# Optimization experiments

Hardware: AMD Instinct MI355X
Metric: run time of the kernel (lower is better)

The kernel has to match this reference:

```python
import jax, jax.numpy as jnp
import numpy as np


def setup_inputs() -> dict:
    key = jax.random.key(0)
    k1, k2 = jax.random.split(key)
    x = jax.random.normal(k1, (32, 112, 112, 64), dtype=jnp.float32)
    kernels = jax.random.normal(k2, (3, 3, 64, 128), dtype=jnp.float32) * 0.05
    biases = jnp.zeros((128,), dtype=jnp.float32)
    return {"x": x, "kernels": kernels, "biases": biases}


def reference(x, kernels, biases):
    # Stride-1 VALID cross-correlation, NHWC input, HWIO kernel -> NHWC output.
    # Matches the original's per-pixel sum(patch * kernel) over all input channels.
    out = jax.lax.conv_general_dilated(
        x, kernels,
        window_strides=(1, 1),
        padding="VALID",
        dimension_numbers=("NHWC", "HWIO", "NHWC"),
    )
    out = out + biases  # broadcast over (B, H_out, W_out, F)
    return jax.nn.relu(out)  # activation=relu per init_kwargs
```

## Files before the change

kernel.cpp:

```cpp
#include <hip/hip_runtime.h>
#include <hip/hip_bf16.h>

typedef __attribute__((ext_vector_type(4))) float f32x4;
typedef __attribute__((ext_vector_type(8))) short bf16x8;
typedef __attribute__((ext_vector_type(8))) unsigned short u16x8;
typedef __attribute__((ext_vector_type(4))) unsigned int u32x4;

#define HH 112
#define WW 112
#define CIN 64
#define COUT 128
#define HOUT 110
#define WOUT 110
#define MTOT 387200
#define NWG 3025
#define NXCD 8
#define XNE 25690112

__device__ __forceinline__ unsigned short f2bf(float f) {
  unsigned int x = __float_as_uint(f);
  x += 0x7fffu + ((x >> 16) & 1u);
  return (unsigned short)(x >> 16);
}

__device__ __forceinline__ unsigned int cvt2(float lo, float hi) {
  union { __hip_bfloat162 h; unsigned int u; } cv;
  cv.h = __float22bfloat162_rn(float2{lo, hi});
  return cv.u;
}

__device__ __forceinline__ void gload16(const unsigned short* g, unsigned short* l) {
  __builtin_amdgcn_global_load_lds(
      (const __attribute__((address_space(1))) void*)g,
      (__attribute__((address_space(3))) void*)l, 16, 0, 0);
}

__global__ __launch_bounds__(256)
void cvt_x_kernel(const float* __restrict__ x, unsigned short* __restrict__ xb) {
  const int t = blockIdx.x * 256 + threadIdx.x;
  const f32x4* s = (const f32x4*)x + (size_t)t * 2;
  f32x4 a = s[0], b = s[1];
  u32x4 v;
  v[0] = cvt2(a[0], a[1]); v[1] = cvt2(a[2], a[3]);
  v[2] = cvt2(b[0], b[1]); v[3] = cvt2(b[2], b[3]);
  ((u32x4*)xb)[t] = v;
}

__global__ void prepack_b_kernel(const float* __restrict__ kern,
                                 unsigned short* __restrict__ bt) {
  int idx = blockIdx.x * 256 + threadIdx.x;
  if (idx >= 9 * 8192) return;
  int tap = idx >> 13;
  int rem = idx & 8191;
  int co = rem >> 6;
  int e = rem & 63;
  int ci = ((e * 2) ^ ((co & 7) << 4)) >> 1;
  bt[idx] = f2bf(kern[(tap * 64 + ci) * COUT + co]);
}

__global__ __launch_bounds__(512, 4)
void conv_dma_kernel(const unsigned short* __restrict__ xb,
                     const unsigned short* __restrict__ bt,
                     const float* __restrict__ bias,
                     float* __restrict__ out) {
  __shared__ __align__(16) unsigned short As[2][8192];
  __shared__ __align__(16) unsigned short Bs[2][8192];

  const int tid = threadIdx.x;
  const int lane = tid & 63;
  const int wid = tid >> 6;

  const int bid = blockIdx.x;
  const int q = NWG / NXCD, r = NWG % NXCD;
  const int xcd = bid % NXCD, i8 = bid / NXCD;
  const int wg = (xcd < r ? xcd * (q + 1) : r * (q + 1) + (xcd - r) * q) + i8;
  const int m0 = wg * 128;

  int aoff[2];
  const int obase = wid * 2048 + lane * 16;
#pragma unroll
  for (int j = 0; j < 2; ++j) {
    const int o = obase + j * 1024;
    const int rr = o >> 7;
    const int ss = (o >> 4) & 7;
    const int sp = ss ^ (rr & 7);
    const int m = m0 + rr;
    const int wo = m % WOUT;
    const int t1 = m / WOUT;
    const int ho = t1 % HOUT;
    const int bb = t1 / HOUT;
    aoff[j] = (((bb * HH) + ho) * WW + wo) * CIN + sp * 8;
  }
  const int ldsw0 = wid * 1024;
  const int ldsw1 = wid * 1024 + 512;
  const int blin0 = ldsw0 + lane * 8;
  const int blin1 = ldsw1 + lane * 8;

  const int wm = wid >> 1;
  const int wn = wid & 1;
  const int l16 = lane & 15;
  const int lk = lane >> 4;
  const int swzR = (l16 & 7) << 4;

  const int aroff0 = (wm * 32 + 0 + l16) * 64;
  const int aroff1 = (wm * 32 + 16 + l16) * 64;
  const int broff0 = (wn * 64 + 0 + l16) * 64;
  const int broff1 = (wn * 64 + 16 + l16) * 64;
  const int broff2 = (wn * 64 + 32 + l16) * 64;
  const int broff3 = (wn * 64 + 48 + l16) * 64;

  f32x4 acc[2][4];
#pragma unroll
  for (int i = 0; i < 2; ++i)
#pragma unroll
    for (int j = 0; j < 4; ++j)
      acc[i][j] = (f32x4){0.f, 0.f, 0.f, 0.f};

  gload16(xb + aoff[0], &As[0][ldsw0]);
  gload16(xb + aoff[1], &As[0][ldsw1]);
  gload16(bt + blin0, &Bs[0][ldsw0]);
  gload16(bt + blin1, &Bs[0][ldsw1]);
  __syncthreads();

#pragma unroll
  for (int kk = 0; kk < 9; ++kk) {
    const int cur = kk & 1;
    const int nxt = cur ^ 1;

    if (kk < 8) {
      const int kn = kk + 1;
      const int kh = kn / 3;
      const int kw = kn - kh * 3;
      const int te = (kh * WW + kw) * CIN;
      const int tb = kn * 8192;
      gload16(xb + aoff[0] + te, &As[nxt][ldsw0]);
      gload16(xb + aoff[1] + te, &As[nxt][ldsw1]);
      gload16(bt + tb + blin0, &Bs[nxt][ldsw0]);
      gload16(bt + tb + blin1, &Bs[nxt][ldsw1]);
    }

    const unsigned short* Ac = As[cur];
    const unsigned short* Bc = Bs[cur];
#pragma unroll
    for (int ks = 0; ks < 2; ++ks) {
      const int cbs = ((ks * 64 + lk * 16) ^ swzR) >> 1;
      bf16x8 a0 = *(const bf16x8*)(Ac + aroff0 + cbs);
      bf16x8 a1 = *(const bf16x8*)(Ac + aroff1 + cbs);
      bf16x8 b0 = *(const bf16x8*)(Bc + broff0 + cbs);
      bf16x8 b1 = *(const bf16x8*)(Bc + broff1 + cbs);
      bf16x8 b2 = *(const bf16x8*)(Bc + broff2 + cbs);
      bf16x8 b3 = *(const bf16x8*)(Bc + broff3 + cbs);
      acc[0][0] = __builtin_amdgcn_mfma_f32_16x16x32_bf16(a0, b0, acc[0][0], 0, 0, 0);
      acc[0][1] = __builtin_amdgcn_mfma_f32_16x16x32_bf16(a0, b1, acc[0][1], 0, 0, 0);
      acc[0][2] = __builtin_amdgcn_mfma_f32_16x16x32_bf16(a0, b2, acc[0][2], 0, 0, 0);
      acc[0][3] = __builtin_amdgcn_mfma_f32_16x16x32_bf16(a0, b3, acc[0][3], 0, 0, 0);
      acc[1][0] = __builtin_amdgcn_mfma_f32_16x16x32_bf16(a1, b0, acc[1][0], 0, 0, 0);
      acc[1][1] = __builtin_amdgcn_mfma_f32_16x16x32_bf16(a1, b1, acc[1][1], 0, 0, 0);
      acc[1][2] = __builtin_amdgcn_mfma_f32_16x16x32_bf16(a1, b2, acc[1][2], 0, 0, 0);
      acc[1][3] = __builtin_amdgcn_mfma_f32_16x16x32_bf16(a1, b3, acc[1][3], 0, 0, 0);
    }

    __syncthreads();
  }

  const int ncol = wn * 64 + l16;
  const float bv0 = bias[ncol + 0];
  const float bv1 = bias[ncol + 16];
  const float bv2 = bias[ncol + 32];
  const float bv3 = bias[ncol + 48];
  const int mrow0 = m0 + wm * 32 + lk * 4;
#pragma unroll
  for (int mf = 0; mf < 2; ++mf) {
#pragma unroll
    for (int j = 0; j < 4; ++j) {
      const int row = mrow0 + mf * 16 + j;
      float* orow = out + (size_t)row * COUT + ncol;
      orow[0]  = fmaxf(acc[mf][0][j] + bv0, 0.f);
      orow[16] = fmaxf(acc[mf][1][j] + bv1, 0.f);
      orow[32] = fmaxf(acc[mf][2][j] + bv2, 0.f);
      orow[48] = fmaxf(acc[mf][3][j] + bv3, 0.f);
    }
  }
}

__global__ __launch_bounds__(512)
void conv_fallback_kernel(const float* __restrict__ x,
                          const float* __restrict__ kern,
                          const float* __restrict__ bias,
                          float* __restrict__ out) {
  __shared__ __align__(16) unsigned short As[2][128 * 64];
  __shared__ __align__(16) unsigned short Bs[2][128 * 64];

  const int tid = threadIdx.x;
  const int m0 = blockIdx.x * 128;

  const int sr = tid >> 2;
  const int sc = tid & 3;
  const int m = m0 + sr;
  const int wo = m % WOUT;
  const int t1 = m / WOUT;
  const int ho = t1 % HOUT;
  const int b = t1 / HOUT;
  const float* xrow = x + (((b * HH) + ho) * WW + wo) * CIN + sc * 16;
  const int swzS = (sr & 7) << 4;
  const int awoff0 = sr * 64 + ((((sc * 32) + 0) ^ swzS) >> 1);
  const int awoff1 = sr * 64 + ((((sc * 32) + 16) ^ swzS) >> 1);

  const int bci = tid >> 3;
  const int bco = (tid & 7) * 16;

  const int lane = tid & 63;
  const int wid = tid >> 6;
  const int wm = wid >> 1;
  const int wn = wid & 1;
  const int l16 = lane & 15;
  const int lk = lane >> 4;
  const int swzR = (l16 & 7) << 4;

  const int aroff0 = (wm * 32 + 0 + l16) * 64;
  const int aroff1 = (wm * 32 + 16 + l16) * 64;
  const int broff0 = (wn * 64 + 0 + l16) * 64;
  const int broff1 = (wn * 64 + 16 + l16) * 64;
  const int broff2 = (wn * 64 + 32 + l16) * 64;
  const int broff3 = (wn * 64 + 48 + l16) * 64;

  f32x4 acc[2][4];
#pragma unroll
  for (int i = 0; i < 2; ++i)
#pragma unroll
    for (int j = 0; j < 4; ++j)
      acc[i][j] = (f32x4){0.f, 0.f, 0.f, 0.f};

  {
    f32x4 f0 = *(const f32x4*)(xrow + 0);
    f32x4 f1 = *(const f32x4*)(xrow + 4);
    f32x4 f2 = *(const f32x4*)(xrow + 8);
    f32x4 f3 = *(const f32x4*)(xrow + 12);
    u32x4 va, vb;
    va[0] = cvt2(f0[0], f0[1]); va[1] = cvt2(f0[2], f0[3]);
    va[2] = cvt2(f1[0], f1[1]); va[3] = cvt2(f1[2], f1[3]);
    vb[0] = cvt2(f2[0], f2[1]); vb[1] = cvt2(f2[2], f2[3]);
    vb[2] = cvt2(f3[0], f3[1]); vb[3] = cvt2(f3[2], f3[3]);
    *(u32x4*)(As[0] + awoff0) = va;
    *(u32x4*)(As[0] + awoff1) = vb;
    const float* kslab = kern + bci * COUT + bco;
    f32x4 g0 = *(const f32x4*)(kslab + 0);
    f32x4 g1 = *(const f32x4*)(kslab + 4);
    f32x4 g2 = *(const f32x4*)(kslab + 8);
    f32x4 g3 = *(const f32x4*)(kslab + 12);
#pragma unroll
    for (int j = 0; j < 4; ++j) {
      int c0 = bco + j;
      Bs[0][c0 * 64 + (((bci * 2) ^ ((c0 & 7) << 4)) >> 1)] = f2bf(g0[j]);
      int c1 = bco + 4 + j;
      Bs[0][c1 * 64 + (((bci * 2) ^ ((c1 & 7) << 4)) >> 1)] = f2bf(g1[j]);
      int c2 = bco + 8 + j;
      Bs[0][c2 * 64 + (((bci * 2) ^ ((c2 & 7) << 4)) >> 1)] = f2bf(g2[j]);
      int c3 = bco + 12 + j;
      Bs[0][c3 * 64 + (((bci * 2) ^ ((c3 & 7) << 4)) >> 1)] = f2bf(g3[j]);
    }
  }

#pragma unroll
  for (int kk = 0; kk < 9; ++kk) {
    const int cur = kk & 1;
    const int nxt = cur ^ 1;

    f32x4 g0, g1, g2, g3;
    f32x4 h0, h1, h2, h3;
    if (kk < 8) {
      const int kn = kk + 1;
      const int kh2 = kn / 3;
      const int kw2 = kn - kh2 * 3;
      const float* src = xrow + (kh2 * WW + kw2) * CIN;
      g0 = *(const f32x4*)(src + 0);
      g1 = *(const f32x4*)(src + 4);
      g2 = *(const f32x4*)(src + 8);
      g3 = *(const f32x4*)(src + 12);
      const float* kslab = kern + (kn * 64 + bci) * COUT + bco;
      h0 = *(const f32x4*)(kslab + 0);
      h1 = *(const f32x4*)(kslab + 4);
      h2 = *(const f32x4*)(kslab + 8);
      h3 = *(const f32x4*)(kslab + 12);
    }

    __syncthreads();

    const unsigned short* Ac = As[cur];
    const unsigned short* Bc = Bs[cur];
#pragma unroll
    for (int ks = 0; ks < 2; ++ks) {
      const int cbs = ((ks * 64 + lk * 16) ^ swzR) >> 1;
      bf16x8 a0 = *(const bf16x8*)(Ac + aroff0 + cbs);
      bf16x8 a1 = *(const bf16x8*)(Ac + aroff1 + cbs);
      bf16x8 b0 = *(const bf16x8*)(Bc + broff0 + cbs);
      bf16x8 b1 = *(const bf16x8*)(Bc + broff1 + cbs);
      bf16x8 b2 = *(const bf16x8*)(Bc + broff2 + cbs);
      bf16x8 b3 = *(const bf16x8*)(Bc + broff3 + cbs);
      acc[0][0] = __builtin_amdgcn_mfma_f32_16x16x32_bf16(a0, b0, acc[0][0], 0, 0, 0);
      acc[0][1] = __builtin_amdgcn_mfma_f32_16x16x32_bf16(a0, b1, acc[0][1], 0, 0, 0);
      acc[0][2] = __builtin_amdgcn_mfma_f32_16x16x32_bf16(a0, b2, acc[0][2], 0, 0, 0);
      acc[0][3] = __builtin_amdgcn_mfma_f32_16x16x32_bf16(a0, b3, acc[0][3], 0, 0, 0);
      acc[1][0] = __builtin_amdgcn_mfma_f32_16x16x32_bf16(a1, b0, acc[1][0], 0, 0, 0);
      acc[1][1] = __builtin_amdgcn_mfma_f32_16x16x32_bf16(a1, b1, acc[1][1], 0, 0, 0);
      acc[1][2] = __builtin_amdgcn_mfma_f32_16x16x32_bf16(a1, b2, acc[1][2], 0, 0, 0);
      acc[1][3] = __builtin_amdgcn_mfma_f32_16x16x32_bf16(a1, b3, acc[1][3], 0, 0, 0);
    }

    if (kk < 8) {
      u32x4 va, vb;
      va[0] = cvt2(g0[0], g0[1]); va[1] = cvt2(g0[2], g0[3]);
      va[2] = cvt2(g1[0], g1[1]); va[3] = cvt2(g1[2], g1[3]);
      vb[0] = cvt2(g2[0], g2[1]); vb[1] = cvt2(g2[2], g2[3]);
      vb[2] = cvt2(g3[0], g3[1]); vb[3] = cvt2(g3[2], g3[3]);
      *(u32x4*)(As[nxt] + awoff0) = va;
      *(u32x4*)(As[nxt] + awoff1) = vb;
#pragma unroll
      for (int j = 0; j < 4; ++j) {
        int c0 = bco + j;
        Bs[nxt][c0 * 64 + (((bci * 2) ^ ((c0 & 7) << 4)) >> 1)] = f2bf(h0[j]);
        int c1 = bco + 4 + j;
        Bs[nxt][c1 * 64 + (((bci * 2) ^ ((c1 & 7) << 4)) >> 1)] = f2bf(h1[j]);
        int c2 = bco + 8 + j;
        Bs[nxt][c2 * 64 + (((bci * 2) ^ ((c2 & 7) << 4)) >> 1)] = f2bf(h2[j]);
        int c3 = bco + 12 + j;
        Bs[nxt][c3 * 64 + (((bci * 2) ^ ((c3 & 7) << 4)) >> 1)] = f2bf(h3[j]);
      }
    }
  }

  const int ncol = wn * 64 + l16;
  const float bv0 = bias[ncol + 0];
  const float bv1 = bias[ncol + 16];
  const float bv2 = bias[ncol + 32];
  const float bv3 = bias[ncol + 48];
  const int mrow0 = m0 + wm * 32 + lk * 4;
#pragma unroll
  for (int mf = 0; mf < 2; ++mf) {
#pragma unroll
    for (int j = 0; j < 4; ++j) {
      const int row = mrow0 + mf * 16 + j;
      float* orow = out + (size_t)row * COUT + ncol;
      orow[0]  = fmaxf(acc[mf][0][j] + bv0, 0.f);
      orow[16] = fmaxf(acc[mf][1][j] + bv1, 0.f);
      orow[32] = fmaxf(acc[mf][2][j] + bv2, 0.f);
      orow[48] = fmaxf(acc[mf][3][j] + bv3, 0.f);
    }
  }
}

extern "C" void kernel_launch(void* const* d_in, const int* in_sizes, int n_in,
                              void* d_out, int out_size, void* d_ws, size_t ws_size,
                              hipStream_t stream) {
  const float* x = (const float*)d_in[0];
  const float* kern = (const float*)d_in[1];
  const float* bias = (const float*)d_in[2];
  float* out = (float*)d_out;

  const size_t xb_bytes = (size_t)XNE * 2;
  const size_t bt_bytes = 9 * 8192 * 2;
  if (d_ws != nullptr && ws_size >= xb_bytes + bt_bytes) {
    unsigned short* xb = (unsigned short*)d_ws;
    unsigned short* bt = xb + XNE;
    cvt_x_kernel<<<12544, 256, 0, stream>>>(x, xb);
    prepack_b_kernel<<<288, 256, 0, stream>>>(kern, bt);
    conv_dma_kernel<<<NWG, 512, 0, stream>>>(xb, bt, bias, out);
  } else {
    conv_fallback_kernel<<<NWG, 512, 0, stream>>>(x, kern, bias, out);
  }
}
```

Before: 110.1 us.

## Halve workgroup to 4 waves, each computing a 64x64 tile

The conv workgroup drops from 8 waves to 4 while keeping the same 128x128 output tile, so each wave now computes 64x64 (4x4 MFMA fragments) instead of 32x64. Each thread issues twice as many async global-to-LDS loads per tap. This raises per-wave register reuse of LDS fragments and cuts LDS read traffic per MFMA. The cost is more accumulator registers per thread and fewer waves to hide latency, with launch bounds changed to 256 threads and 2 blocks.

```diff
diff --git a/kernel.cpp b/kernel.cpp
--- a/kernel.cpp
+++ b/kernel.cpp
@@ -58,7 +58,7 @@
   bt[idx] = f2bf(kern[(tap * 64 + ci) * COUT + co]);
 }
 
-__global__ __launch_bounds__(512, 4)
+__global__ __launch_bounds__(256, 2)
 void conv_dma_kernel(const unsigned short* __restrict__ xb,
                      const unsigned short* __restrict__ bt,
                      const float* __restrict__ bias,
@@ -76,11 +76,10 @@
   const int wg = (xcd < r ? xcd * (q + 1) : r * (q + 1) + (xcd - r) * q) + i8;
   const int m0 = wg * 128;
 
-  int aoff[2];
-  const int obase = wid * 2048 + lane * 16;
-#pragma unroll
-  for (int j = 0; j < 2; ++j) {
-    const int o = obase + j * 1024;
+  int aoff[4];
+#pragma unroll
+  for (int j = 0; j < 4; ++j) {
+    const int o = wid * 4096 + j * 1024 + lane * 16;
     const int rr = o >> 7;
     const int ss = (o >> 4) & 7;
     const int sp = ss ^ (rr & 7);
@@ -91,10 +90,12 @@
     const int bb = t1 / HOUT;
     aoff[j] = (((bb * HH) + ho) * WW + wo) * CIN + sp * 8;
   }
-  const int ldsw0 = wid * 1024;
-  const int ldsw1 = wid * 1024 + 512;
-  const int blin0 = ldsw0 + lane * 8;
-  const int blin1 = ldsw1 + lane * 8;
+  int ldsw[4], blin[4];
+#pragma unroll
+  for (int j = 0; j < 4; ++j) {
+    ldsw[j] = wid * 2048 + j * 512;
+    blin[j] = ldsw[j] + lane * 8;
+  }
 
   const int wm = wid >> 1;
   const int wn = wid & 1;
@@ -102,24 +103,25 @@
   const int lk = lane >> 4;
   const int swzR = (l16 & 7) << 4;
 
-  const int aroff0 = (wm * 32 + 0 + l16) * 64;
-  const int aroff1 = (wm * 32 + 16 + l16) * 64;
-  const int broff0 = (wn * 64 + 0 + l16) * 64;
-  const int broff1 = (wn * 64 + 16 + l16) * 64;
-  const int broff2 = (wn * 64 + 32 + l16) * 64;
-  const int broff3 = (wn * 64 + 48 + l16) * 64;
-
-  f32x4 acc[2][4];
-#pragma unroll
-  for (int i = 0; i < 2; ++i)
+  int ar[4], br[4];
+#pragma unroll
+  for (int f = 0; f < 4; ++f) {
+    ar[f] = (wm * 64 + f * 16 + l16) * 64;
+    br[f] = (wn * 64 + f * 16 + l16) * 64;
+  }
+
+  f32x4 acc[4][4];
+#pragma unroll
+  for (int i = 0; i < 4; ++i)
 #pragma unroll
     for (int j = 0; j < 4; ++j)
       acc[i][j] = (f32x4){0.f, 0.f, 0.f, 0.f};
 
-  gload16(xb + aoff[0], &As[0][ldsw0]);
-  gload16(xb + aoff[1], &As[0][ldsw1]);
-  gload16(bt + blin0, &Bs[0][ldsw0]);
-  gload16(bt + blin1, &Bs[0][ldsw1]);
+#pragma unroll
+  for (int j = 0; j < 4; ++j) {
+    gload16(xb + aoff[j], &As[0][ldsw[j]]);
+    gload16(bt + blin[j], &Bs[0][ldsw[j]]);
+  }
   __syncthreads();
 
 #pragma unroll
@@ -133,10 +135,11 @@
       const int kw = kn - kh * 3;
       const int te = (kh * WW + kw) * CIN;
       const int tb = kn * 8192;
-      gload16(xb + aoff[0] + te, &As[nxt][ldsw0]);
-      gload16(xb + aoff[1] + te, &As[nxt][ldsw1]);
-      gload16(bt + tb + blin0, &Bs[nxt][ldsw0]);
-      gload16(bt + tb + blin1, &Bs[nxt][ldsw1]);
+#pragma unroll
+      for (int j = 0; j < 4; ++j) {
+        gload16(xb + aoff[j] + te, &As[nxt][ldsw[j]]);
+        gload16(bt + tb + blin[j], &Bs[nxt][ldsw[j]]);
+      }
     }
 
     const unsigned short* Ac = As[cur];
@@ -144,12 +147,14 @@
 #pragma unroll
     for (int ks = 0; ks < 2; ++ks) {
       const int cbs = ((ks * 64 + lk * 16) ^ swzR) >> 1;
-      bf16x8 a0 = *(const bf16x8*)(Ac + aroff0 + cbs);
-      bf16x8 a1 = *(const bf16x8*)(Ac + aroff1 + cbs);
-      bf16x8 b0 = *(const bf16x8*)(Bc + broff0 + cbs);
-      bf16x8 b1 = *(const bf16x8*)(Bc + broff1 + cbs);
-      bf16x8 b2 = *(const bf16x8*)(Bc + broff2 + cbs);
-      bf16x8 b3 = *(const bf16x8*)(Bc + broff3 + cbs);
+      bf16x8 a0 = *(const bf16x8*)(Ac + ar[0] + cbs);
+      bf16x8 a1 = *(const bf16x8*)(Ac + ar[1] + cbs);
+      bf16x8 a2 = *(const bf16x8*)(Ac + ar[2] + cbs);
+      bf16x8 a3 = *(const bf16x8*)(Ac + ar[3] + cbs);
+      bf16x8 b0 = *(const bf16x8*)(Bc + br[0] + cbs);
+      bf16x8 b1 = *(const bf16x8*)(Bc + br[1] + cbs);
+      bf16x8 b2 = *(const bf16x8*)(Bc + br[2] + cbs);
+      bf16x8 b3 = *(const bf16x8*)(Bc + br[3] + cbs);
       acc[0][0] = __builtin_amdgcn_mfma_f32_16x16x32_bf16(a0, b0, acc[0][0], 0, 0, 0);
       acc[0][1] = __builtin_amdgcn_mfma_f32_16x16x32_bf16(a0, b1, acc[0][1], 0, 0, 0);
       acc[0][2] = __builtin_amdgcn_mfma_f32_16x16x32_bf16(a0, b2, acc[0][2], 0, 0, 0);
@@ -158,6 +163,14 @@
       acc[1][1] = __builtin_amdgcn_mfma_f32_16x16x32_bf16(a1, b1, acc[1][1], 0, 0, 0);
       acc[1][2] = __builtin_amdgcn_mfma_f32_16x16x32_bf16(a1, b2, acc[1][2], 0, 0, 0);
       acc[1][3] = __builtin_amdgcn_mfma_f32_16x16x32_bf16(a1, b3, acc[1][3], 0, 0, 0);
+      acc[2][0] = __builtin_amdgcn_mfma_f32_16x16x32_bf16(a2, b0, acc[2][0], 0, 0, 0);
+      acc[2][1] = __builtin_amdgcn_mfma_f32_16x16x32_bf16(a2, b1, acc[2][1], 0, 0, 0);
+      acc[2][2] = __builtin_amdgcn_mfma_f32_16x16x32_bf16(a2, b2, acc[2][2], 0, 0, 0);
+      acc[2][3] = __builtin_amdgcn_mfma_f32_16x16x32_bf16(a2, b3, acc[2][3], 0, 0, 0);
+      acc[3][0] = __builtin_amdgcn_mfma_f32_16x16x32_bf16(a3, b0, acc[3][0], 0, 0, 0);
+      acc[3][1] = __builtin_amdgcn_mfma_f32_16x16x32_bf16(a3, b1, acc[3][1], 0, 0, 0);
+      acc[3][2] = __builtin_amdgcn_mfma_f32_16x16x32_bf16(a3, b2, acc[3][2], 0, 0, 0);
+      acc[3][3] = __builtin_amdgcn_mfma_f32_16x16x32_bf16(a3, b3, acc[3][3], 0, 0, 0);
     }
 
     __syncthreads();
@@ -168,13 +181,12 @@
   const float bv1 = bias[ncol + 16];
   const float bv2 = bias[ncol + 32];
   const float bv3 = bias[ncol + 48];
-  const int mrow0 = m0 + wm * 32 + lk * 4;
-#pragma unroll
-  for (int mf = 0; mf < 2; ++mf) {
+#pragma unroll
+  for (int mf = 0; mf < 4; ++mf) {
+    const int rbase = m0 + wm * 64 + mf * 16 + lk * 4;
 #pragma unroll
     for (int j = 0; j < 4; ++j) {
-      const int row = mrow0 + mf * 16 + j;
-      float* orow = out + (size_t)row * COUT + ncol;
+      float* orow = out + (size_t)(rbase + j) * COUT + ncol;
       orow[0]  = fmaxf(acc[mf][0][j] + bv0, 0.f);
       orow[16] = fmaxf(acc[mf][1][j] + bv1, 0.f);
       orow[32] = fmaxf(acc[mf][2][j] + bv2, 0.f);
@@ -364,7 +376,7 @@
     unsigned short* bt = xb + XNE;
     cvt_x_kernel<<<12544, 256, 0, stream>>>(x, xb);
     prepack_b_kernel<<<288, 256, 0, stream>>>(kern, bt);
-    conv_dma_kernel<<<NWG, 512, 0, stream>>>(xb, bt, bias, out);
+    conv_dma_kernel<<<NWG, 256, 0, stream>>>(xb, bt, bias, out);
   } else {
     conv_fallback_kernel<<<NWG, 512, 0, stream>>>(x, kern, bias, out);
   }
```

Measured after the change: 117.4 us. +6.7%, slower.

## Load weight fragments directly from global into registers instead of LDS

Applied to the files above, without the earlier changes.

The weight (B) tile is no longer staged through shared memory. Each lane loads its MFMA B fragments straight from the prepacked global buffer into double-buffered registers, and the prepack now uses an unswizzled layout. This halves LDS usage and removes the LDS reads for B, which could allow higher occupancy, and it also drops the final barrier. The cost is more VGPRs (32 extra bf16x8 registers) and uncoalesced-ish per-lane global loads that rely on L2/L1 hits, which may raise register pressure under launch_bounds(512,4).

```diff
diff --git a/kernel.cpp b/kernel.cpp
--- a/kernel.cpp
+++ b/kernel.cpp
@@ -53,8 +53,7 @@
   int tap = idx >> 13;
   int rem = idx & 8191;
   int co = rem >> 6;
-  int e = rem & 63;
-  int ci = ((e * 2) ^ ((co & 7) << 4)) >> 1;
+  int ci = rem & 63;
   bt[idx] = f2bf(kern[(tap * 64 + ci) * COUT + co]);
 }
 
@@ -64,7 +63,6 @@
                      const float* __restrict__ bias,
                      float* __restrict__ out) {
   __shared__ __align__(16) unsigned short As[2][8192];
-  __shared__ __align__(16) unsigned short Bs[2][8192];
 
   const int tid = threadIdx.x;
   const int lane = tid & 63;
@@ -82,8 +80,7 @@
   for (int j = 0; j < 2; ++j) {
     const int o = obase + j * 1024;
     const int rr = o >> 7;
-    const int ss = (o >> 4) & 7;
-    const int sp = ss ^ (rr & 7);
+    const int sp = ((o >> 4) & 7) ^ (rr & 7);
     const int m = m0 + rr;
     const int wo = m % WOUT;
     const int t1 = m / WOUT;
@@ -93,8 +90,6 @@
   }
   const int ldsw0 = wid * 1024;
   const int ldsw1 = wid * 1024 + 512;
-  const int blin0 = ldsw0 + lane * 8;
-  const int blin1 = ldsw1 + lane * 8;
 
   const int wm = wid >> 1;
   const int wn = wid & 1;
@@ -104,10 +99,8 @@
 
   const int aroff0 = (wm * 32 + 0 + l16) * 64;
   const int aroff1 = (wm * 32 + 16 + l16) * 64;
-  const int broff0 = (wn * 64 + 0 + l16) * 64;
-  const int broff1 = (wn * 64 + 16 + l16) * 64;
-  const int broff2 = (wn * 64 + 32 + l16) * 64;
-  const int broff3 = (wn * 64 + 48 + l16) * 64;
+
+  const unsigned short* bq_base = bt + (wn * 64 + l16) * 64 + lk * 8;
 
   f32x4 acc[2][4];
 #pragma unroll
@@ -116,10 +109,15 @@
     for (int j = 0; j < 4; ++j)
       acc[i][j] = (f32x4){0.f, 0.f, 0.f, 0.f};
 
+  bf16x8 bq[2][2][4];
+
   gload16(xb + aoff[0], &As[0][ldsw0]);
   gload16(xb + aoff[1], &As[0][ldsw1]);
-  gload16(bt + blin0, &Bs[0][ldsw0]);
-  gload16(bt + blin1, &Bs[0][ldsw1]);
+#pragma unroll
+  for (int f = 0; f < 4; ++f)
+#pragma unroll
+    for (int ks = 0; ks < 2; ++ks)
+      bq[0][ks][f] = *(const bf16x8*)(bq_base + f * 1024 + ks * 32);
   __syncthreads();
 
 #pragma unroll
@@ -132,35 +130,33 @@
       const int kh = kn / 3;
       const int kw = kn - kh * 3;
       const int te = (kh * WW + kw) * CIN;
-      const int tb = kn * 8192;
       gload16(xb + aoff[0] + te, &As[nxt][ldsw0]);
       gload16(xb + aoff[1] + te, &As[nxt][ldsw1]);
-      gload16(bt + tb + blin0, &Bs[nxt][ldsw0]);
-      gload16(bt + tb + blin1, &Bs[nxt][ldsw1]);
+      const unsigned short* bsrc = bq_base + kn * 8192;
+#pragma unroll
+      for (int f = 0; f < 4; ++f)
+#pragma unroll
+        for (int ks = 0; ks < 2; ++ks)
+          bq[nxt][ks][f] = *(const bf16x8*)(bsrc + f * 1024 + ks * 32);
     }
 
     const unsigned short* Ac = As[cur];
-    const unsigned short* Bc = Bs[cur];
 #pragma unroll
     for (int ks = 0; ks < 2; ++ks) {
       const int cbs = ((ks * 64 + lk * 16) ^ swzR) >> 1;
       bf16x8 a0 = *(const bf16x8*)(Ac + aroff0 + cbs);
       bf16x8 a1 = *(const bf16x8*)(Ac + aroff1 + cbs);
-      bf16x8 b0 = *(const bf16x8*)(Bc + broff0 + cbs);
-      bf16x8 b1 = *(const bf16x8*)(Bc + broff1 + cbs);
-      bf16x8 b2 = *(const bf16x8*)(Bc + broff2 + cbs);
-      bf16x8 b3 = *(const bf16x8*)(Bc + broff3 + cbs);
-      acc[0][0] = __builtin_amdgcn_mfma_f32_16x16x32_bf16(a0, b0, acc[0][0], 0, 0, 0);
-      acc[0][1] = __builtin_amdgcn_mfma_f32_16x16x32_bf16(a0, b1, acc[0][1], 0, 0, 0);
-      acc[0][2] = __builtin_amdgcn_mfma_f32_16x16x32_bf16(a0, b2, acc[0][2], 0, 0, 0);
-      acc[0][3] = __builtin_amdgcn_mfma_f32_16x16x32_bf16(a0, b3, acc[0][3], 0, 0, 0);
-      acc[1][0] = __builtin_amdgcn_mfma_f32_16x16x32_bf16(a1, b0, acc[1][0], 0, 0, 0);
-      acc[1][1] = __builtin_amdgcn_mfma_f32_16x16x32_bf16(a1, b1, acc[1][1], 0, 0, 0);
-      acc[1][2] = __builtin_amdgcn_mfma_f32_16x16x32_bf16(a1, b2, acc[1][2], 0, 0, 0);
-      acc[1][3] = __builtin_amdgcn_mfma_f32_16x16x32_bf16(a1, b3, acc[1][3], 0, 0, 0);
-    }
-
-    __syncthreads();
+      acc[0][0] = __builtin_amdgcn_mfma_f32_16x16x32_bf16(a0, bq[cur][ks][0], acc[0][0], 0, 0, 0);
+      acc[0][1] = __builtin_amdgcn_mfma_f32_16x16x32_bf16(a0, bq[cur][ks][1], acc[0][1], 0, 0, 0);
+      acc[0][2] = __builtin_amdgcn_mfma_f32_16x16x32_bf16(a0, bq[cur][ks][2], acc[0][2], 0, 0, 0);
+      acc[0][3] = __builtin_amdgcn_mfma_f32_16x16x32_bf16(a0, bq[cur][ks][3], acc[0][3], 0, 0, 0);
+      acc[1][0] = __builtin_amdgcn_mfma_f32_16x16x32_bf16(a1, bq[cur][ks][0], acc[1][0], 0, 0, 0);
+      acc[1][1] = __builtin_amdgcn_mfma_f32_16x16x32_bf16(a1, bq[cur][ks][1], acc[1][1], 0, 0, 0);
+      acc[1][2] = __builtin_amdgcn_mfma_f32_16x16x32_bf16(a1, bq[cur][ks][2], acc[1][2], 0, 0, 0);
+      acc[1][3] = __builtin_amdgcn_mfma_f32_16x16x32_bf16(a1, bq[cur][ks][3], acc[1][3], 0, 0, 0);
+    }
+
+    if (kk < 8) __syncthreads();
   }
 
   const int ncol = wn * 64 + l16;
@@ -366,6 +362,6 @@
     prepack_b_kernel<<<288, 256, 0, stream>>>(kern, bt);
     conv_dma_kernel<<<NWG, 512, 0, stream>>>(xb, bt, bias, out);
   } else {
-    conv_fallback_kernel<<<NWG, 512, 0, stream>>>(x, kern, bias, out);
-  }
-}
+    conv_fallback_kernel<<<3025, 512, 0, stream>>>(x, kern, bias, out);
+  }
+}
```

New measurement: 249.5 us. +126.7%, slower.

## Triple-buffer A tiles with vmcnt-based waits and a single barrier per tap

Applied to the files above, without the earlier changes.

The A (activation) tile ring grows from two LDS buffers to three, so the loads for tap k+2 are issued while tap k computes. The B prefetch stays double-buffered. The per-iteration __syncthreads pair becomes one explicit s_waitcnt vmcnt plus s_barrier, which keeps later prefetches in flight instead of draining all outstanding loads. The cost is more LDS per block (48KB), which could lower occupancy, and correctness now depends on the async load counter ordering being right.

```diff
diff --git a/kernel.cpp b/kernel.cpp
--- a/kernel.cpp
+++ b/kernel.cpp
@@ -63,7 +63,7 @@
                      const unsigned short* __restrict__ bt,
                      const float* __restrict__ bias,
                      float* __restrict__ out) {
-  __shared__ __align__(16) unsigned short As[2][8192];
+  __shared__ __align__(16) unsigned short As[3][8192];
   __shared__ __align__(16) unsigned short Bs[2][8192];
 
   const int tid = threadIdx.x;
@@ -82,8 +82,7 @@
   for (int j = 0; j < 2; ++j) {
     const int o = obase + j * 1024;
     const int rr = o >> 7;
-    const int ss = (o >> 4) & 7;
-    const int sp = ss ^ (rr & 7);
+    const int sp = ((o >> 4) & 7) ^ (rr & 7);
     const int m = m0 + rr;
     const int wo = m % WOUT;
     const int t1 = m / WOUT;
@@ -116,31 +115,46 @@
     for (int j = 0; j < 4; ++j)
       acc[i][j] = (f32x4){0.f, 0.f, 0.f, 0.f};
 
+  auto tapoff = [](int tap) {
+    const int kh = tap / 3;
+    const int kw = tap - kh * 3;
+    return (kh * WW + kw) * CIN;
+  };
+
+  gload16(bt + blin0, &Bs[0][ldsw0]);
+  gload16(bt + blin1, &Bs[0][ldsw1]);
   gload16(xb + aoff[0], &As[0][ldsw0]);
   gload16(xb + aoff[1], &As[0][ldsw1]);
-  gload16(bt + blin0, &Bs[0][ldsw0]);
-  gload16(bt + blin1, &Bs[0][ldsw1]);
-  __syncthreads();
+  {
+    const int te = tapoff(1);
+    gload16(xb + aoff[0] + te, &As[1][ldsw0]);
+    gload16(xb + aoff[1] + te, &As[1][ldsw1]);
+  }
 
 #pragma unroll
   for (int kk = 0; kk < 9; ++kk) {
-    const int cur = kk & 1;
-    const int nxt = cur ^ 1;
-
     if (kk < 8) {
-      const int kn = kk + 1;
-      const int kh = kn / 3;
-      const int kw = kn - kh * 3;
-      const int te = (kh * WW + kw) * CIN;
-      const int tb = kn * 8192;
-      gload16(xb + aoff[0] + te, &As[nxt][ldsw0]);
-      gload16(xb + aoff[1] + te, &As[nxt][ldsw1]);
-      gload16(bt + tb + blin0, &Bs[nxt][ldsw0]);
-      gload16(bt + tb + blin1, &Bs[nxt][ldsw1]);
-    }
-
-    const unsigned short* Ac = As[cur];
-    const unsigned short* Bc = Bs[cur];
+      asm volatile("s_waitcnt vmcnt(2)" ::: "memory");
+    } else {
+      asm volatile("s_waitcnt vmcnt(0)" ::: "memory");
+    }
+    __builtin_amdgcn_s_barrier();
+
+    if (kk < 8) {
+      const int tb = (kk + 1) * 8192;
+      unsigned short* bd = Bs[(kk + 1) & 1];
+      gload16(bt + tb + blin0, bd + ldsw0);
+      gload16(bt + tb + blin1, bd + ldsw1);
+    }
+    if (kk < 7) {
+      const int te = tapoff(kk + 2);
+      unsigned short* ad = As[(kk + 2) % 3];
+      gload16(xb + aoff[0] + te, ad + ldsw0);
+      gload16(xb + aoff[1] + te, ad + ldsw1);
+    }
+
+    const unsigned short* Ac = As[kk % 3];
+    const unsigned short* Bc = Bs[kk & 1];
 #pragma unroll
     for (int ks = 0; ks < 2; ++ks) {
       const int cbs = ((ks * 64 + lk * 16) ^ swzR) >> 1;
@@ -159,8 +173,6 @@
       acc[1][2] = __builtin_amdgcn_mfma_f32_16x16x32_bf16(a1, b2, acc[1][2], 0, 0, 0);
       acc[1][3] = __builtin_amdgcn_mfma_f32_16x16x32_bf16(a1, b3, acc[1][3], 0, 0, 0);
     }
-
-    __syncthreads();
   }
 
   const int ncol = wn * 64 + l16;
@@ -366,6 +378,6 @@
     prepack_b_kernel<<<288, 256, 0, stream>>>(kern, bt);
     conv_dma_kernel<<<NWG, 512, 0, stream>>>(xb, bt, bias, out);
   } else {
-    conv_fallback_kernel<<<NWG, 512, 0, stream>>>(x, kern, bias, out);
-  }
-}
+    conv_fallback_kernel<<<3025, 512, 0, stream>>>(x, kern, bias, out);
+  }
+}
```

Measured after the change: 105.3 us. 4.3% less time.
